# Performance work log

Measured on AMD Instinct MI355X. Metric: run time of the kernel, lower is better.

Reference implementation:

```python
import jax, jax.numpy as jnp
import numpy as np
from jax import lax

EPS = 1e-12  # F.normalize default eps
NUM_HEADS = 3
TEMP = 1.0

def setup_inputs() -> dict:
    key = jax.random.key(0)
    ks = jax.random.split(key, 7)
    b, c, h, w = 4, 96, 256, 256
    s = 0.02
    return {
        'x': jax.random.normal(ks[0], (b, c, h, w), jnp.float32),
        'qkv_w': jax.random.normal(ks[1], (3 * c, c), jnp.float32) * s,
        'qkv_b': jax.random.normal(ks[2], (3 * c,), jnp.float32) * s,
        'dw_w': jax.random.normal(ks[3], (3 * c, 1, 3, 3), jnp.float32) * s,
        'dw_b': jax.random.normal(ks[4], (3 * c,), jnp.float32) * s,
        'proj_w': jax.random.normal(ks[5], (c, c), jnp.float32) * s,
        'proj_b': jax.random.normal(ks[6], (c,), jnp.float32) * s,
    }

def _l2norm(t):
    # F.normalize over last dim: t / max(||t||, eps)
    n = jnp.sqrt(jnp.sum(t * t, axis=-1, keepdims=True))
    return t / jnp.maximum(n, EPS)

def reference(x, qkv_w, qkv_b, dw_w, dw_b, proj_w, proj_b):
    b, c, h, w = x.shape
    head = NUM_HEADS
    # 1x1 conv (pointwise) -> [b, 3c, h, w]
    qkv = jnp.einsum('oc,bchw->bohw', qkv_w, x) + qkv_b[None, :, None, None]
    # 3x3 depthwise conv, padding=1
    qkv = lax.conv_general_dilated(
        qkv, dw_w, window_strides=(1, 1), padding='SAME',
        feature_group_count=3 * c,
        dimension_numbers=('NCHW', 'OIHW', 'NCHW')) + dw_b[None, :, None, None]
    q, k, v = jnp.split(qkv, 3, axis=1)
    # b (head hc) h w -> b head hc (h w)
    def to_heads(t):
        return t.reshape(b, head, c // head, h * w)
    q, k, v = to_heads(q), to_heads(k), to_heads(v)
    q = _l2norm(q)
    k = _l2norm(k)
    # channel-wise attention scores: [b, head, hc, hc]
    attn = jnp.einsum('bhcn,bhdn->bhcd', q, k) * TEMP
    attn = jax.nn.softmax(attn, axis=-1)
    out = jnp.einsum('bhcd,bhdn->bhcn', attn, v)  # [b, head, hc, hw]
    out = out.reshape(b, c, h, w)
    out = jnp.einsum('oc,bchw->bohw', proj_w, out) + proj_b[None, :, None, None]
    return (out, attn)
```

## Files before the change

### kernel.cpp

```cpp
#include <hip/hip_runtime.h>
#include <hip/hip_bf16.h>

#define B_  4
#define C_  96
#define H_  256
#define W_  256
#define N_  (H_*W_)
#define C3_ 288
#define HEAD_ 3
#define HC_ 32
#define EPS_ 1e-12f
#define XP_ 104
#define SPLITS_ 128

typedef __attribute__((ext_vector_type(8))) short short8;
typedef __attribute__((ext_vector_type(4))) float f32x4;

__device__ __forceinline__ unsigned short f2bf(float f) {
  unsigned u = __float_as_uint(f);
  u += 0x7fffu + ((u >> 16) & 1u);
  return (unsigned short)(u >> 16);
}
__device__ __forceinline__ float bf2f(unsigned short h) {
  return __uint_as_float((unsigned)h << 16);
}
__device__ __forceinline__ float bf_lo(unsigned u) { return __uint_as_float(u << 16); }
__device__ __forceinline__ float bf_hi(unsigned u) { return __uint_as_float(u & 0xffff0000u); }
__device__ __forceinline__ unsigned pack_bf(float a, float b) {
  return (unsigned)f2bf(a) | ((unsigned)f2bf(b) << 16);
}

__global__ __launch_bounds__(512) void k1_mfma(
    const float* __restrict__ x, const float* __restrict__ wsrc,
    const float* __restrict__ bias, unsigned short* __restrict__ out) {
  __shared__ unsigned short Wl[C3_ * XP_];
  __shared__ float Bl[C3_];
  const int tid = threadIdx.x;
  const int b = blockIdx.y;
  for (int i = tid; i < C3_ * C_; i += 512)
    Wl[(i / 96) * XP_ + (i % 96)] = f2bf(wsrc[i]);
  for (int i = tid; i < C3_; i += 512) Bl[i] = bias[i];
  __syncthreads();
  const int lane = tid & 63;
  const int wv = tid >> 6;
  const int l15 = lane & 15, quad = lane >> 4;
  const int gpix = blockIdx.x * 128 + wv * 16 + l15;
  const float* xcol = x + (size_t)b * C_ * N_ + gpix;
  short8 bfr[3];
#pragma unroll
  for (int kc = 0; kc < 3; ++kc) {
#pragma unroll
    for (int u = 0; u < 8; ++u)
      bfr[kc][u] = (short)f2bf(xcol[(size_t)(kc * 32 + quad * 8 + u) * N_]);
  }
  f32x4 acc[18];
#pragma unroll
  for (int m = 0; m < 18; ++m) acc[m] = (f32x4){0.f, 0.f, 0.f, 0.f};
#pragma unroll
  for (int m = 0; m < 18; ++m) {
#pragma unroll
    for (int kc = 0; kc < 3; ++kc) {
      const short8 afr = *reinterpret_cast<const short8*>(
          &Wl[(m * 16 + l15) * XP_ + kc * 32 + quad * 8]);
      acc[m] = __builtin_amdgcn_mfma_f32_16x16x32_bf16(afr, bfr[kc], acc[m], 0, 0, 0);
    }
  }
  unsigned short* ob = out + (size_t)b * C3_ * N_ + gpix;
#pragma unroll
  for (int m = 0; m < 18; ++m) {
    const int chb = m * 16 + quad * 4;
#pragma unroll
    for (int r = 0; r < 4; ++r)
      ob[(size_t)(chb + r) * N_] = f2bf(acc[m][r] + Bl[chb + r]);
  }
}

__global__ __launch_bounds__(256) void k_dw_reg(
    unsigned short* a, const float* __restrict__ w9,
    const float* __restrict__ bias, float* __restrict__ inv) {
  const int bc = blockIdx.x;
  const int ch = bc % C3_;
  unsigned short* p = a + (size_t)bc * N_;
  const int tid = threadIdx.x;
  const int tr = tid >> 5;
  const int tc = tid & 31;
  const int x0 = tc * 8;
  const int y0 = tr * 32;
  float wv[9];
#pragma unroll
  for (int i = 0; i < 9; ++i) wv[i] = w9[ch * 9 + i];
  const float bv = bias[ch];

  auto load_row = [&](int y, float* d) {
    if ((unsigned)y >= 256u) {
#pragma unroll
      for (int j = 0; j < 10; ++j) d[j] = 0.f;
      return;
    }
    const unsigned short* rp = p + (size_t)y * W_;
    const uint4 u = *reinterpret_cast<const uint4*>(rp + x0);
    d[1] = bf_lo(u.x); d[2] = bf_hi(u.x); d[3] = bf_lo(u.y); d[4] = bf_hi(u.y);
    d[5] = bf_lo(u.z); d[6] = bf_hi(u.z); d[7] = bf_lo(u.w); d[8] = bf_hi(u.w);
    d[0] = (tc > 0) ? bf2f(rp[x0 - 1]) : 0.f;
    d[9] = (tc < 31) ? bf2f(rp[x0 + 8]) : 0.f;
  };

  float rm[10], rc[10], rn[10], rb[10];
  load_row(y0 - 1, rm);
  load_row(y0, rc);
  load_row(y0 + 1, rn);
  load_row(y0 + 32, rb);
  __syncthreads();

  float ss = 0.f;
  for (int y = y0; y < y0 + 32; ++y) {
    float o[8];
#pragma unroll
    for (int j = 0; j < 8; ++j) {
      o[j] = bv + wv[0] * rm[j] + wv[1] * rm[j + 1] + wv[2] * rm[j + 2]
                + wv[3] * rc[j] + wv[4] * rc[j + 1] + wv[5] * rc[j + 2]
                + wv[6] * rn[j] + wv[7] * rn[j + 1] + wv[8] * rn[j + 2];
      ss += o[j] * o[j];
    }
    uint4 st;
    st.x = pack_bf(o[0], o[1]); st.y = pack_bf(o[2], o[3]);
    st.z = pack_bf(o[4], o[5]); st.w = pack_bf(o[6], o[7]);
    *reinterpret_cast<uint4*>(p + (size_t)y * W_ + x0) = st;
#pragma unroll
    for (int j = 0; j < 10; ++j) { rm[j] = rc[j]; rc[j] = rn[j]; }
    const int ny = y + 2;
    if (ny <= y0 + 31) {
      load_row(ny, rn);
    } else if (ny == y0 + 32) {
#pragma unroll
      for (int j = 0; j < 10; ++j) rn[j] = rb[j];
    }
  }
#pragma unroll
  for (int off = 32; off > 0; off >>= 1) ss += __shfl_down(ss, off, 64);
  __shared__ float red[4];
  if ((tid & 63) == 0) red[tid >> 6] = ss;
  __syncthreads();
  if (tid == 0 && ch < 192) {
    const float t = red[0] + red[1] + red[2] + red[3];
    const int b = bc / C3_;
    inv[b * 192 + ch] = 1.0f / fmaxf(sqrtf(t), EPS_);
  }
}

__global__ __launch_bounds__(256) void k_attn_mfma(
    const unsigned short* __restrict__ dw, float* __restrict__ part) {
  const int tid = threadIdx.x;
  const int lane = tid & 63;
  const int wv = tid >> 6;
  const int i0 = (wv >> 1) * 16, j0 = (wv & 1) * 16;
  const int h = blockIdx.y, b = blockIdx.z;
  const int n0 = blockIdx.x * (N_ / SPLITS_);
  const int l15 = lane & 15, quad = lane >> 4;
  const unsigned short* qrow =
      dw + ((size_t)(b * C3_ + h * HC_ + i0 + l15)) * N_ + n0 + quad * 8;
  const unsigned short* krow =
      dw + ((size_t)(b * C3_ + C_ + h * HC_ + j0 + l15)) * N_ + n0 + quad * 8;
  f32x4 acc = (f32x4){0.f, 0.f, 0.f, 0.f};
#pragma unroll 8
  for (int s = 0; s < N_ / SPLITS_; s += 32) {
    const short8 af = *reinterpret_cast<const short8*>(qrow + s);
    const short8 bf = *reinterpret_cast<const short8*>(krow + s);
    acc = __builtin_amdgcn_mfma_f32_16x16x32_bf16(af, bf, acc, 0, 0, 0);
  }
  float* pp = part + (size_t)blockIdx.x * (B_ * HEAD_ * 1024)
                   + ((size_t)(b * HEAD_ + h)) * 1024;
#pragma unroll
  for (int r = 0; r < 4; ++r)
    pp[(i0 + quad * 4 + r) * 32 + j0 + l15] = acc[r];
}

__global__ __launch_bounds__(256) void k_softmax(
    const float* __restrict__ part, const float* __restrict__ inv,
    float* __restrict__ attn_out) {
  __shared__ float red[2][4][32];
  const int tid = threadIdx.x;
  {
    const int r2 = tid >> 7;
    const int loc = tid & 127;
    const int sg = loc >> 5;
    const int j = loc & 31;
    const int R = blockIdx.x * 2 + r2;
    float v = 0.f;
#pragma unroll 8
    for (int s = sg; s < SPLITS_; s += 4)
      v += part[(size_t)s * (B_ * HEAD_ * 1024) + R * 32 + j];
    red[r2][sg][j] = v;
  }
  __syncthreads();
  if (tid < 64) {
    const int r2 = tid >> 5, j = tid & 31;
    const int R = blockIdx.x * 2 + r2;
    const int b = R / 96, rem = R % 96;
    const int h = rem / 32, i = rem % 32;
    float v = red[r2][0][j] + red[r2][1][j] + red[r2][2][j] + red[r2][3][j];
    v *= inv[b * 192 + h * 32 + i] * inv[b * 192 + 96 + h * 32 + j];
    float m = v;
#pragma unroll
    for (int off = 16; off > 0; off >>= 1) m = fmaxf(m, __shfl_xor(m, off, 32));
    const float e = __expf(v - m);
    float s = e;
#pragma unroll
    for (int off = 16; off > 0; off >>= 1) s += __shfl_xor(s, off, 32);
    attn_out[R * 32 + j] = e / s;
  }
}

__global__ __launch_bounds__(256) void k_M(
    const float* __restrict__ attn, const float* __restrict__ proj_w,
    unsigned short* __restrict__ Mbf) {
  const int b = blockIdx.x, h = blockIdx.y;
  const int tid = threadIdx.x;
  __shared__ float As[1024];
  __shared__ float Pw[C_ * 32];
  for (int l = tid; l < 1024; l += 256)
    As[l] = attn[((size_t)b * HEAD_ + h) * 1024 + l];
  for (int l = tid; l < C_ * 32; l += 256)
    Pw[l] = proj_w[(l >> 5) * C_ + h * 32 + (l & 31)];
  __syncthreads();
  for (int e = tid; e < C_ * 32; e += 256) {
    const int o = e >> 5, j = e & 31;
    float s = 0.f;
#pragma unroll
    for (int i = 0; i < 32; ++i) s += Pw[o * 32 + i] * As[i * 32 + j];
    Mbf[(size_t)b * C_ * C_ + o * C_ + h * 32 + j] = f2bf(s);
  }
}

__global__ __launch_bounds__(256) void k7_mfma(
    const unsigned short* __restrict__ A ,
    const unsigned short* __restrict__ Mbf,
    const float* __restrict__ bias, float* __restrict__ out) {
  const int tid = threadIdx.x;
  const int b = blockIdx.y;
  const int lane = tid & 63;
  const int wv = tid >> 6;
  const int l15 = lane & 15, quad = lane >> 4;
  const int gpix = blockIdx.x * 64 + wv * 16 + l15;
  const unsigned short* vcol = A + ((size_t)(b * C3_ + 2 * C_)) * N_ + gpix;
  const unsigned short* Mb = Mbf + (size_t)b * C_ * C_;
  short8 bfr[3];
#pragma unroll
  for (int kc = 0; kc < 3; ++kc) {
#pragma unroll
    for (int u = 0; u < 8; ++u)
      bfr[kc][u] = (short)vcol[(size_t)(kc * 32 + quad * 8 + u) * N_];
  }
  f32x4 acc[6];
#pragma unroll
  for (int m = 0; m < 6; ++m) acc[m] = (f32x4){0.f, 0.f, 0.f, 0.f};
#pragma unroll
  for (int m = 0; m < 6; ++m) {
#pragma unroll
    for (int kc = 0; kc < 3; ++kc) {
      const short8 afr = *reinterpret_cast<const short8*>(
          Mb + (m * 16 + l15) * C_ + kc * 32 + quad * 8);
      acc[m] = __builtin_amdgcn_mfma_f32_16x16x32_bf16(afr, bfr[kc], acc[m], 0, 0, 0);
    }
  }
  float* ob = out + (size_t)b * C_ * N_ + gpix;
#pragma unroll
  for (int m = 0; m < 6; ++m) {
    const int chb = m * 16 + quad * 4;
#pragma unroll
    for (int r = 0; r < 4; ++r)
      ob[(size_t)(chb + r) * N_] = acc[m][r] + bias[chb + r];
  }
}

extern "C" void kernel_launch(void* const* d_in, const int* in_sizes, int n_in,
                              void* d_out, int out_size, void* d_ws, size_t ws_size,
                              hipStream_t stream) {
  const float* x      = (const float*)d_in[0];
  const float* qkv_w  = (const float*)d_in[1];
  const float* qkv_b  = (const float*)d_in[2];
  const float* dw_w   = (const float*)d_in[3];
  const float* dw_b   = (const float*)d_in[4];
  const float* proj_w = (const float*)d_in[5];
  const float* proj_b = (const float*)d_in[6];

  float* out      = (float*)d_out;
  float* attn_out = out + (size_t)B_ * C_ * N_;

  unsigned short* A = (unsigned short*)d_ws;
  float* inv   = (float*)(A + (size_t)B_ * C3_ * N_);
  float* part  = inv + 768;
  unsigned short* Mbf = (unsigned short*)(part + SPLITS_ * B_ * HEAD_ * 1024);

  k1_mfma<<<dim3(N_ / 128, B_), 512, 0, stream>>>(x, qkv_w, qkv_b, A);
  k_dw_reg<<<B_ * C3_, 256, 0, stream>>>(A, dw_w, dw_b, inv);
  k_attn_mfma<<<dim3(SPLITS_, HEAD_, B_), 256, 0, stream>>>(A, part);
  k_softmax<<<192, 256, 0, stream>>>(part, inv, attn_out);
  k_M<<<dim3(B_, HEAD_), 256, 0, stream>>>(attn_out, proj_w, Mbf);
  k7_mfma<<<dim3(N_ / 64, B_), 256, 0, stream>>>(A, Mbf, proj_b, out);
}
```

Baseline: 347.2 us.

## Fuse depthwise conv of Q/K into Gram-matrix MFMA kernel, split V dwconv

The Q and K depthwise 3x3 convolutions are now computed on the fly inside a new kernel that feeds the results straight into the QK^T MFMA accumulation. The dwconv output for Q/K is no longer written back to memory, and the separate attention partial-product kernel is gone. Sum-of-squares for L2 normalisation is accumulated with atomics into a zeroed buffer, and the normalisation is done in the softmax kernel. V gets its own dwconv kernel. The projection kernel swaps MFMA operand roles so it can store results as float4 vectors. The trade-off is that the fused kernel recomputes neighbouring rows for each 8-row band, and the split count drops from 128 to 32.

Result: slower. 551.9 us (+58.9%).

```diff
diff --git a/kernel.cpp b/kernel.cpp
--- a/kernel.cpp
+++ b/kernel.cpp
@@ -11,7 +11,7 @@
 #define HC_ 32
 #define EPS_ 1e-12f
 #define XP_ 104
-#define SPLITS_ 128
+#define SPLITS_ 32
 
 typedef __attribute__((ext_vector_type(8))) short short8;
 typedef __attribute__((ext_vector_type(4))) float f32x4;
@@ -28,6 +28,11 @@
 __device__ __forceinline__ float bf_hi(unsigned u) { return __uint_as_float(u & 0xffff0000u); }
 __device__ __forceinline__ unsigned pack_bf(float a, float b) {
   return (unsigned)f2bf(a) | ((unsigned)f2bf(b) << 16);
+}
+__device__ __forceinline__ unsigned cvt_pk(float lo, float hi) {
+  unsigned r;
+  asm("v_cvt_pk_bf16_f32 %0, %1, %2" : "=v"(r) : "v"(lo), "v"(hi));
+  return r;
 }
 
 __global__ __launch_bounds__(512) void k1_mfma(
@@ -75,12 +80,108 @@
   }
 }
 
-__global__ __launch_bounds__(256) void k_dw_reg(
+__device__ __forceinline__ void load10v(const unsigned short* p, int y, int x0,
+                                        float* d) {
+  if ((unsigned)y >= 256u) {
+#pragma unroll
+    for (int j = 0; j < 10; ++j) d[j] = 0.f;
+    return;
+  }
+  const unsigned short* rp = p + (size_t)y * W_;
+  const uint4 u = *reinterpret_cast<const uint4*>(rp + x0);
+  d[1] = bf_lo(u.x); d[2] = bf_hi(u.x); d[3] = bf_lo(u.y); d[4] = bf_hi(u.y);
+  d[5] = bf_lo(u.z); d[6] = bf_hi(u.z); d[7] = bf_lo(u.w); d[8] = bf_hi(u.w);
+  d[0] = (x0 > 0)   ? bf2f(rp[x0 - 1]) : 0.f;
+  d[9] = (x0 < 248) ? bf2f(rp[x0 + 8]) : 0.f;
+}
+
+__device__ __forceinline__ short8 dw8(const unsigned short* p, int y, int x0,
+                                      const float* t, float& ss) {
+  float a[10], c[10], d[10];
+  load10v(p, y - 1, x0, a);
+  load10v(p, y,     x0, c);
+  load10v(p, y + 1, x0, d);
+  float o[8];
+#pragma unroll
+  for (int j = 0; j < 8; ++j) {
+    o[j] = t[9] + t[0] * a[j] + t[1] * a[j + 1] + t[2] * a[j + 2]
+                + t[3] * c[j] + t[4] * c[j + 1] + t[5] * c[j + 2]
+                + t[6] * d[j] + t[7] * d[j + 1] + t[8] * d[j + 2];
+    ss += o[j] * o[j];
+  }
+  union { short8 s; unsigned u[4]; } r;
+  r.u[0] = cvt_pk(o[0], o[1]); r.u[1] = cvt_pk(o[2], o[3]);
+  r.u[2] = cvt_pk(o[4], o[5]); r.u[3] = cvt_pk(o[6], o[7]);
+  return r.s;
+}
+
+__global__ __launch_bounds__(512) void k_dwqk(
+    const unsigned short* __restrict__ A, const float* __restrict__ w9,
+    const float* __restrict__ bias, float* __restrict__ part,
+    float* __restrict__ ssbuf) {
+  __shared__ float taps[64][10];
+  __shared__ float redbuf[8][1024];
+  const int band = blockIdx.x, h = blockIdx.y, b = blockIdx.z;
+  const int tid = threadIdx.x;
+  for (int i = tid; i < 640; i += 512) {
+    const int cl = i / 10, k = i % 10;
+    const int ach = (cl < 32) ? (h * HC_ + cl) : (C_ + h * HC_ + (cl - 32));
+    taps[cl][k] = (k < 9) ? w9[ach * 9 + k] : bias[ach];
+  }
+  __syncthreads();
+  const int wv = tid >> 6;
+  const int lane = tid & 63;
+  const int l15 = lane & 15, quad = lane >> 4;
+  const int x0 = wv * 32 + quad * 8;
+  const int y0 = band * 8;
+  const unsigned short* pQ0 = A + ((size_t)(b * C3_ + h * HC_ + l15)) * N_;
+  const unsigned short* pQ1 = pQ0 + (size_t)16 * N_;
+  const unsigned short* pK0 = A + ((size_t)(b * C3_ + C_ + h * HC_ + l15)) * N_;
+  const unsigned short* pK1 = pK0 + (size_t)16 * N_;
+  float ss0 = 0.f, ss1 = 0.f, ss2 = 0.f, ss3 = 0.f;
+  f32x4 acc[2][2];
+#pragma unroll
+  for (int qi = 0; qi < 2; ++qi)
+#pragma unroll
+    for (int kj = 0; kj < 2; ++kj) acc[qi][kj] = (f32x4){0.f, 0.f, 0.f, 0.f};
+  for (int y = y0; y < y0 + 8; ++y) {
+    const short8 fq0 = dw8(pQ0, y, x0, &taps[l15][0],      ss0);
+    const short8 fq1 = dw8(pQ1, y, x0, &taps[l15 + 16][0], ss1);
+    const short8 fk0 = dw8(pK0, y, x0, &taps[32 + l15][0], ss2);
+    const short8 fk1 = dw8(pK1, y, x0, &taps[48 + l15][0], ss3);
+    acc[0][0] = __builtin_amdgcn_mfma_f32_16x16x32_bf16(fq0, fk0, acc[0][0], 0, 0, 0);
+    acc[0][1] = __builtin_amdgcn_mfma_f32_16x16x32_bf16(fq0, fk1, acc[0][1], 0, 0, 0);
+    acc[1][0] = __builtin_amdgcn_mfma_f32_16x16x32_bf16(fq1, fk0, acc[1][0], 0, 0, 0);
+    acc[1][1] = __builtin_amdgcn_mfma_f32_16x16x32_bf16(fq1, fk1, acc[1][1], 0, 0, 0);
+  }
+  atomicAdd(&ssbuf[b * 192 + h * HC_ + l15],            ss0);
+  atomicAdd(&ssbuf[b * 192 + h * HC_ + l15 + 16],       ss1);
+  atomicAdd(&ssbuf[b * 192 + 96 + h * HC_ + l15],       ss2);
+  atomicAdd(&ssbuf[b * 192 + 96 + h * HC_ + l15 + 16],  ss3);
+#pragma unroll
+  for (int qi = 0; qi < 2; ++qi)
+#pragma unroll
+    for (int kj = 0; kj < 2; ++kj)
+#pragma unroll
+      for (int r = 0; r < 4; ++r)
+        redbuf[wv][(qi * 16 + quad * 4 + r) * 32 + kj * 16 + l15] = acc[qi][kj][r];
+  __syncthreads();
+  float* pp = part + (size_t)band * (B_ * HEAD_ * 1024) + ((size_t)(b * HEAD_ + h)) * 1024;
+  for (int e = tid; e < 1024; e += 512) {
+    float s = 0.f;
+#pragma unroll
+    for (int w = 0; w < 8; ++w) s += redbuf[w][e];
+    pp[e] = s;
+  }
+}
+
+__global__ __launch_bounds__(256) void k_dwv(
     unsigned short* a, const float* __restrict__ w9,
-    const float* __restrict__ bias, float* __restrict__ inv) {
+    const float* __restrict__ bias) {
   const int bc = blockIdx.x;
-  const int ch = bc % C3_;
-  unsigned short* p = a + (size_t)bc * N_;
+  const int b = bc / 96, cv = bc % 96;
+  const int ch = 2 * C_ + cv;
+  unsigned short* p = a + ((size_t)(b * C3_ + ch)) * N_;
   const int tid = threadIdx.x;
   const int tr = tid >> 5;
   const int tc = tid & 31;
@@ -112,7 +213,6 @@
   load_row(y0 + 32, rb);
   __syncthreads();
 
-  float ss = 0.f;
   for (int y = y0; y < y0 + 32; ++y) {
     float o[8];
 #pragma unroll
@@ -120,7 +220,6 @@
       o[j] = bv + wv[0] * rm[j] + wv[1] * rm[j + 1] + wv[2] * rm[j + 2]
                 + wv[3] * rc[j] + wv[4] * rc[j + 1] + wv[5] * rc[j + 2]
                 + wv[6] * rn[j] + wv[7] * rn[j + 1] + wv[8] * rn[j + 2];
-      ss += o[j] * o[j];
     }
     uint4 st;
     st.x = pack_bf(o[0], o[1]); st.y = pack_bf(o[2], o[3]);
@@ -136,47 +235,10 @@
       for (int j = 0; j < 10; ++j) rn[j] = rb[j];
     }
   }
-#pragma unroll
-  for (int off = 32; off > 0; off >>= 1) ss += __shfl_down(ss, off, 64);
-  __shared__ float red[4];
-  if ((tid & 63) == 0) red[tid >> 6] = ss;
-  __syncthreads();
-  if (tid == 0 && ch < 192) {
-    const float t = red[0] + red[1] + red[2] + red[3];
-    const int b = bc / C3_;
-    inv[b * 192 + ch] = 1.0f / fmaxf(sqrtf(t), EPS_);
-  }
-}
-
-__global__ __launch_bounds__(256) void k_attn_mfma(
-    const unsigned short* __restrict__ dw, float* __restrict__ part) {
-  const int tid = threadIdx.x;
-  const int lane = tid & 63;
-  const int wv = tid >> 6;
-  const int i0 = (wv >> 1) * 16, j0 = (wv & 1) * 16;
-  const int h = blockIdx.y, b = blockIdx.z;
-  const int n0 = blockIdx.x * (N_ / SPLITS_);
-  const int l15 = lane & 15, quad = lane >> 4;
-  const unsigned short* qrow =
-      dw + ((size_t)(b * C3_ + h * HC_ + i0 + l15)) * N_ + n0 + quad * 8;
-  const unsigned short* krow =
-      dw + ((size_t)(b * C3_ + C_ + h * HC_ + j0 + l15)) * N_ + n0 + quad * 8;
-  f32x4 acc = (f32x4){0.f, 0.f, 0.f, 0.f};
-#pragma unroll 8
-  for (int s = 0; s < N_ / SPLITS_; s += 32) {
-    const short8 af = *reinterpret_cast<const short8*>(qrow + s);
-    const short8 bf = *reinterpret_cast<const short8*>(krow + s);
-    acc = __builtin_amdgcn_mfma_f32_16x16x32_bf16(af, bf, acc, 0, 0, 0);
-  }
-  float* pp = part + (size_t)blockIdx.x * (B_ * HEAD_ * 1024)
-                   + ((size_t)(b * HEAD_ + h)) * 1024;
-#pragma unroll
-  for (int r = 0; r < 4; ++r)
-    pp[(i0 + quad * 4 + r) * 32 + j0 + l15] = acc[r];
 }
 
 __global__ __launch_bounds__(256) void k_softmax(
-    const float* __restrict__ part, const float* __restrict__ inv,
+    const float* __restrict__ part, const float* __restrict__ ssbuf,
     float* __restrict__ attn_out) {
   __shared__ float red[2][4][32];
   const int tid = threadIdx.x;
@@ -199,7 +261,9 @@
     const int b = R / 96, rem = R % 96;
     const int h = rem / 32, i = rem % 32;
     float v = red[r2][0][j] + red[r2][1][j] + red[r2][2][j] + red[r2][3][j];
-    v *= inv[b * 192 + h * 32 + i] * inv[b * 192 + 96 + h * 32 + j];
+    const float ssq = ssbuf[b * 192 + h * 32 + i];
+    const float ssk = ssbuf[b * 192 + 96 + h * 32 + j];
+    v *= (1.0f / fmaxf(sqrtf(ssq), EPS_)) * (1.0f / fmaxf(sqrtf(ssk), EPS_));
     float m = v;
 #pragma unroll
     for (int off = 16; off > 0; off >>= 1) m = fmaxf(m, __shfl_xor(m, off, 32));
@@ -241,15 +305,15 @@
   const int lane = tid & 63;
   const int wv = tid >> 6;
   const int l15 = lane & 15, quad = lane >> 4;
-  const int gpix = blockIdx.x * 64 + wv * 16 + l15;
-  const unsigned short* vcol = A + ((size_t)(b * C3_ + 2 * C_)) * N_ + gpix;
+  const int pixbase = blockIdx.x * 64 + wv * 16;
+  const unsigned short* vcol = A + ((size_t)(b * C3_ + 2 * C_)) * N_ + pixbase + l15;
   const unsigned short* Mb = Mbf + (size_t)b * C_ * C_;
-  short8 bfr[3];
+  short8 afr[3];
 #pragma unroll
   for (int kc = 0; kc < 3; ++kc) {
 #pragma unroll
     for (int u = 0; u < 8; ++u)
-      bfr[kc][u] = (short)vcol[(size_t)(kc * 32 + quad * 8 + u) * N_];
+      afr[kc][u] = (short)vcol[(size_t)(kc * 32 + quad * 8 + u) * N_];
   }
   f32x4 acc[6];
 #pragma unroll
@@ -258,18 +322,19 @@
   for (int m = 0; m < 6; ++m) {
 #pragma unroll
     for (int kc = 0; kc < 3; ++kc) {
-      const short8 afr = *reinterpret_cast<const short8*>(
+      const short8 mfr = *reinterpret_cast<const short8*>(
           Mb + (m * 16 + l15) * C_ + kc * 32 + quad * 8);
-      acc[m] = __builtin_amdgcn_mfma_f32_16x16x32_bf16(afr, bfr[kc], acc[m], 0, 0, 0);
-    }
-  }
-  float* ob = out + (size_t)b * C_ * N_ + gpix;
+      acc[m] = __builtin_amdgcn_mfma_f32_16x16x32_bf16(afr[kc], mfr, acc[m], 0, 0, 0);
+    }
+  }
+  float* ob = out + (size_t)b * C_ * N_ + pixbase + quad * 4;
 #pragma unroll
   for (int m = 0; m < 6; ++m) {
-    const int chb = m * 16 + quad * 4;
-#pragma unroll
-    for (int r = 0; r < 4; ++r)
-      ob[(size_t)(chb + r) * N_] = acc[m][r] + bias[chb + r];
+    const float bv = bias[m * 16 + l15];
+    f32x4 st;
+#pragma unroll
+    for (int r = 0; r < 4; ++r) st[r] = acc[m][r] + bv;
+    *reinterpret_cast<f32x4*>(ob + (size_t)(m * 16 + l15) * N_) = st;
   }
 }
 
@@ -288,14 +353,15 @@
   float* attn_out = out + (size_t)B_ * C_ * N_;
 
   unsigned short* A = (unsigned short*)d_ws;
-  float* inv   = (float*)(A + (size_t)B_ * C3_ * N_);
-  float* part  = inv + 768;
-  unsigned short* Mbf = (unsigned short*)(part + SPLITS_ * B_ * HEAD_ * 1024);
-
+  float* ssbuf = (float*)(A + (size_t)B_ * C3_ * N_);
+  float* part  = ssbuf + 768;
+  unsigned short* Mbf = (unsigned short*)(part + (size_t)SPLITS_ * B_ * HEAD_ * 1024);
+
+  hipMemsetAsync(ssbuf, 0, 768 * sizeof(float), stream);
   k1_mfma<<<dim3(N_ / 128, B_), 512, 0, stream>>>(x, qkv_w, qkv_b, A);
-  k_dw_reg<<<B_ * C3_, 256, 0, stream>>>(A, dw_w, dw_b, inv);
-  k_attn_mfma<<<dim3(SPLITS_, HEAD_, B_), 256, 0, stream>>>(A, part);
-  k_softmax<<<192, 256, 0, stream>>>(part, inv, attn_out);
+  k_dwqk<<<dim3(SPLITS_, HEAD_, B_), 512, 0, stream>>>(A, dw_w, dw_b, part, ssbuf);
+  k_dwv<<<B_ * 96, 256, 0, stream>>>(A, dw_w, dw_b);
+  k_softmax<<<192, 256, 0, stream>>>(part, ssbuf, attn_out);
   k_M<<<dim3(B_, HEAD_), 256, 0, stream>>>(attn_out, proj_w, Mbf);
   k7_mfma<<<dim3(N_ / 64, B_), 256, 0, stream>>>(A, Mbf, proj_b, out);
 }
```
